# Optimization experiments

Measured on AMD Instinct MI355X. Metric: run time of the kernel, lower is better.

Reference implementation:

```python
import jax, jax.numpy as jnp
import numpy as np

BJORCK_BETA = 0.5
BJORCK_ITERS = 25

def bjorck_orthonormalize(w, iters=BJORCK_ITERS):
    # Order-2 Bjorck iteration (beta must be 0.5):
    # w <- 15/8 * w - 5/4 * w (w^T w) + 3/8 * w (w^T w)^2
    def body(i, w):
        wtw = w.T @ w                     # [out, out] on the thin side
        wtw2 = wtw @ wtw
        return 1.875 * w - 1.25 * (w @ wtw) + 0.375 * (w @ wtw2)
    return jax.lax.fori_loop(0, iters, body, w)

def setup_inputs() -> dict:
    key = jax.random.key(0)
    k1, k2, k3 = jax.random.split(key, 3)
    N, D_IN, D_OUT = 8192, 512, 256
    x = jax.random.normal(k1, (N, D_IN), dtype=jnp.float32)
    adj = jax.random.uniform(k2, (N, N), dtype=jnp.float32)
    weight = jax.random.normal(k3, (D_OUT, D_IN), dtype=jnp.float32) / np.sqrt(D_IN)
    return {"x": x, "adj": adj, "weight": weight}

def reference(x, adj, weight):
    # safe Bjorck scaling: sqrt(rows * cols) of the weight (shape-only constant)
    scaling = jnp.sqrt(jnp.float32(weight.shape[0] * weight.shape[1]))
    # orthonormalize weight.T / scaling, then transpose back -> [out, in]
    ortho_w = bjorck_orthonormalize(weight.T / scaling).T
    h = x @ ortho_w.T                      # [N, out] == F.linear(x, ortho_w)
    return jax.nn.relu(adj @ h)            # [N, out]
```

## Files before the change

### kernel.cpp

```cpp
#include <hip/hip_runtime.h>

typedef __attribute__((ext_vector_type(8))) short bf16x8;
typedef __attribute__((ext_vector_type(4))) short bf16x4;
typedef __attribute__((ext_vector_type(4))) float f32x4;

__device__ __forceinline__ unsigned short f2bf(float x){
  unsigned u = __float_as_uint(x);
  u = (u + 0x7fffu + ((u >> 16) & 1u)) >> 16;
  return (unsigned short)u;
}

__device__ __forceinline__ bf16x8 cvtpack8(float4 a, float4 b){
  union { bf16x8 v; unsigned short u[8]; } p;
  p.u[0] = f2bf(a.x); p.u[1] = f2bf(a.y); p.u[2] = f2bf(a.z); p.u[3] = f2bf(a.w);
  p.u[4] = f2bf(b.x); p.u[5] = f2bf(b.y); p.u[6] = f2bf(b.z); p.u[7] = f2bf(b.w);
  return p.v;
}

__device__ __forceinline__ void gload16(const void* g, void* l){
  __builtin_amdgcn_global_load_lds(
      (const __attribute__((address_space(1))) unsigned int*)g,
      (__attribute__((address_space(3))) unsigned int*)l, 16, 0, 0);
}


__global__ __launch_bounds__(256) void kzero(float* __restrict__ G0, float* __restrict__ n2){
  int b = blockIdx.x;
  if (b < 256) G0[b * 256 + threadIdx.x] = 0.0f;
  else if (threadIdx.x == 0) *n2 = 0.0f;
}


__global__ __launch_bounds__(256) void knorm(const float* __restrict__ wt, float* __restrict__ n2){
  int t = blockIdx.x * 256 + threadIdx.x;
  float4 v = reinterpret_cast<const float4*>(wt)[t];
  float s = v.x*v.x + v.y*v.y + v.z*v.z + v.w*v.w;
  #pragma unroll
  for (int o = 32; o > 0; o >>= 1) s += __shfl_down(s, o, 64);
  __shared__ float red[4];
  if ((threadIdx.x & 63) == 0) red[threadIdx.x >> 6] = s;
  __syncthreads();
  if (threadIdx.x == 0) atomicAdd(n2, red[0] + red[1] + red[2] + red[3]);
}

__global__ __launch_bounds__(256) void kinit(const float* __restrict__ wt, const float* __restrict__ n2,
                                             float* __restrict__ W){
  int c = blockIdx.x;
  int r = threadIdx.x;
  float s = rsqrtf(*n2) * (1.0f / 0.3f);
  W[(size_t)r * 256 + c]         = wt[(size_t)c * 512 + r] * s;
  W[(size_t)(r + 256) * 256 + c] = wt[(size_t)c * 512 + r + 256] * s;
}

__global__ __launch_bounds__(256) void kgram2(const float* __restrict__ W, float* __restrict__ G){
  __shared__ __align__(16) float Wi[64][32];
  __shared__ __align__(16) float Wj[64][32];
  const int t = threadIdx.x;
  const int i0 = blockIdx.y * 32, j0 = blockIdx.x * 32, k0 = blockIdx.z * 64;
  const int lr = t >> 3, lc = (t & 7) * 4;
  #pragma unroll
  for (int p = 0; p < 2; ++p){
    int r = lr + p * 32;
    *reinterpret_cast<float4*>(&Wi[r][lc]) =
        *reinterpret_cast<const float4*>(&W[(size_t)(k0 + r) * 256 + i0 + lc]);
    *reinterpret_cast<float4*>(&Wj[r][lc]) =
        *reinterpret_cast<const float4*>(&W[(size_t)(k0 + r) * 256 + j0 + lc]);
  }
  __syncthreads();
  const int tx = t & 31, iy = t >> 5;
  float g0 = 0, g1 = 0, g2 = 0, g3 = 0;
  #pragma unroll 8
  for (int k = 0; k < 64; ++k){
    float wj = Wj[k][tx];
    float4 wi = *reinterpret_cast<const float4*>(&Wi[k][iy * 4]);
    g0 = fmaf(wi.x, wj, g0); g1 = fmaf(wi.y, wj, g1);
    g2 = fmaf(wi.z, wj, g2); g3 = fmaf(wi.w, wj, g3);
  }
  float* gp = &G[(size_t)(i0 + iy * 4) * 256 + j0 + tx];
  atomicAdd(gp,       g0); atomicAdd(gp + 256, g1);
  atomicAdd(gp + 512, g2); atomicAdd(gp + 768, g3);
}

__global__ __launch_bounds__(512) void kupdate2(float* __restrict__ W, const float* __restrict__ G,
    float* __restrict__ Gnext, float ca, float cb, float cc, int last,
    unsigned short* __restrict__ WT2){
  __shared__ float wr[2][256], yl[2][256];
  const int t = threadIdx.x;
  const int c = t & 255, row = t >> 8;
  const int r = blockIdx.x * 2 + row;
  wr[row][c] = W[(size_t)r * 256 + c];
  __syncthreads();
  float y = 0;
  #pragma unroll 8
  for (int k = 0; k < 256; ++k)
    y = fmaf(wr[row][k], G[(size_t)k * 256 + c], y);
  yl[row][c] = y;
  __syncthreads();
  float d = 0;
  #pragma unroll 8
  for (int k = 0; k < 256; ++k)
    d = fmaf(yl[row][k], G[(size_t)k * 256 + c], d);
  float nw = ca * wr[row][c] + cb * y + cc * d;
  W[(size_t)r * 256 + c] = nw;
  if (r < 256) Gnext[(size_t)r * 256 + c] = 0.0f;
  if (last){
    size_t e = (size_t)(r >> 5) * 8192 + (size_t)((r >> 3) & 3) * 2048 + (size_t)c * 8 + (r & 7);
    WT2[e] = f2bf(nw);
  }
}


template<int KDIM, int KS, int EPI>
__global__ __launch_bounds__(256) void kgemmS(const float* __restrict__ A,
    const unsigned short* __restrict__ B, void* __restrict__ Cout){
  __shared__ __align__(16) unsigned short As[2][4096];
  __shared__ __align__(16) unsigned short Bs[2][8192];

  const int t = threadIdx.x;
  const int w = t >> 6, lane = t & 63;
  const int rlo = lane & 15, l16 = lane >> 4;
  const int kp = (KS > 1) ? (int)(blockIdx.x % KS) : 0;
  const int rb = (KS > 1) ? (int)(blockIdx.x / KS) : (int)blockIdx.x;
  constexpr int KLOC = KDIM / KS;
  constexpr int NS = KLOC / 32;
  const int kbase = kp * KLOC;

  const int arow = t >> 1, akh = t & 1;
  const float* astg = A + (size_t)(rb * 128 + arow) * KDIM + kbase + akh * 16;
  const int aswz = (arow >> 1) & 3;
  const int ab0 = arow * 64 + ((2 * akh)     ^ aswz) * 16;
  const int ab1 = arow * 64 + ((2 * akh + 1) ^ aswz) * 16;
  const unsigned short* bstg = B + (size_t)(kbase >> 5) * 8192 + w * 2048 + lane * 8;

  f32x4 acc[2][16];
  #pragma unroll
  for (int mf = 0; mf < 2; ++mf)
    #pragma unroll
    for (int nf = 0; nf < 16; ++nf){
      acc[mf][nf][0] = 0.f; acc[mf][nf][1] = 0.f;
      acc[mf][nf][2] = 0.f; acc[mf][nf][3] = 0.f;
    }

  float4 q0, q1, q2, q3;
#define LOADA(S) { const float* p_ = astg + (size_t)(S) * 32; \
    q0 = *reinterpret_cast<const float4*>(p_); \
    q1 = *reinterpret_cast<const float4*>(p_ + 4); \
    q2 = *reinterpret_cast<const float4*>(p_ + 8); \
    q3 = *reinterpret_cast<const float4*>(p_ + 12); }
#define WRITEA(BUF) { char* b_ = reinterpret_cast<char*>(&As[BUF][0]); \
    *reinterpret_cast<bf16x8*>(b_ + ab0) = cvtpack8(q0, q1); \
    *reinterpret_cast<bf16x8*>(b_ + ab1) = cvtpack8(q2, q3); }
#define STAGE_B(BUF, S) { \
    _Pragma("unroll") \
    for (int i = 0; i < 4; ++i) \
      gload16(bstg + (size_t)(S) * 8192 + i * 512, &Bs[BUF][w * 2048 + i * 512]); }
#define COMPUTE(BUF) { \
    bf16x8 afr[2]; \
    const char* ab_ = reinterpret_cast<const char*>(&As[BUF][0]); \
    _Pragma("unroll") \
    for (int mf = 0; mf < 2; ++mf){ \
      int row = w * 32 + mf * 16 + rlo; \
      afr[mf] = *reinterpret_cast<const bf16x8*>( \
          ab_ + row * 64 + ((l16 ^ ((row >> 1) & 3)) * 16)); \
    } \
    _Pragma("unroll") \
    for (int nf = 0; nf < 16; ++nf){ \
      bf16x8 bf_ = *reinterpret_cast<const bf16x8*>(&Bs[BUF][l16 * 2048 + (nf * 16 + rlo) * 8]); \
      acc[0][nf] = __builtin_amdgcn_mfma_f32_16x16x32_bf16(afr[0], bf_, acc[0][nf], 0, 0, 0); \
      acc[1][nf] = __builtin_amdgcn_mfma_f32_16x16x32_bf16(afr[1], bf_, acc[1][nf], 0, 0, 0); \
    } }

  STAGE_B(0, 0);
  LOADA(0);
  WRITEA(0);
  __syncthreads();

  #pragma unroll 1
  for (int s = 0; s < NS; ++s){
    const int cur = s & 1;
    if (s + 1 < NS){ STAGE_B(cur ^ 1, s + 1); LOADA(s + 1); }
    COMPUTE(cur);
    if (s + 1 < NS) WRITEA(cur ^ 1);
    __syncthreads();
  }
#undef LOADA
#undef WRITEA
#undef STAGE_B
#undef COMPUTE

  if constexpr (EPI == 0){
    unsigned short* H = reinterpret_cast<unsigned short*>(Cout);
    #pragma unroll
    for (int mf = 0; mf < 2; ++mf)
      #pragma unroll
      for (int nf = 0; nf < 16; ++nf){
        int c  = nf * 16 + rlo;
        int m0 = rb * 128 + w * 32 + mf * 16 + (l16 << 2);
        size_t e = (size_t)(m0 >> 5) * 8192 + (size_t)((m0 >> 3) & 3) * 2048
                 + (size_t)c * 8 + (m0 & 7);
        union { bf16x4 v; unsigned short u[4]; } p;
        p.u[0] = f2bf(acc[mf][nf][0]);
        p.u[1] = f2bf(acc[mf][nf][1]);
        p.u[2] = f2bf(acc[mf][nf][2]);
        p.u[3] = f2bf(acc[mf][nf][3]);
        *reinterpret_cast<bf16x4*>(&H[e]) = p.v;
      }
  } else {
    float* O = reinterpret_cast<float*>(Cout) + (size_t)kp * 8192 * 256;
    #pragma unroll
    for (int mf = 0; mf < 2; ++mf)
      #pragma unroll
      for (int nf = 0; nf < 16; ++nf){
        int c  = nf * 16 + rlo;
        int m0 = rb * 128 + w * 32 + mf * 16 + (l16 << 2);
        #pragma unroll
        for (int j = 0; j < 4; ++j)
          O[(size_t)(m0 + j) * 256 + c] = acc[mf][nf][j];
      }
  }
}

__global__ __launch_bounds__(256) void kreduce8(const float* __restrict__ P, float* __restrict__ O){
  size_t i = (size_t)blockIdx.x * 256 + threadIdx.x;
  const float4* p = reinterpret_cast<const float4*>(P);
  float4 r = p[i];
  #pragma unroll
  for (int q = 1; q < 8; ++q){
    float4 b = p[i + (size_t)q * 524288];
    r.x += b.x; r.y += b.y; r.z += b.z; r.w += b.w;
  }
  r.x = fmaxf(r.x, 0.f); r.y = fmaxf(r.y, 0.f);
  r.z = fmaxf(r.z, 0.f); r.w = fmaxf(r.w, 0.f);
  reinterpret_cast<float4*>(O)[i] = r;
}


extern "C" void kernel_launch(void* const* d_in, const int* in_sizes, int n_in,
                              void* d_out, int out_size, void* d_ws, size_t ws_size,
                              hipStream_t stream) {
  const float* x   = (const float*)d_in[0];
  const float* adj = (const float*)d_in[1];
  const float* wt  = (const float*)d_in[2];
  float* out = (float*)d_out;

  char* ws = (char*)d_ws;
  float* n2            = (float*)ws;
  float* W             = (float*)(ws + 4096);
  float* G0            = (float*)(ws + 4096 + 524288);
  float* G1            = (float*)(ws + 4096 + 524288 + 262144);
  unsigned short* WT2  = (unsigned short*)(ws + 4096 + 524288 + 2*262144);
  unsigned short* HT2  = (unsigned short*)(ws + 4096 + 524288 + 3*262144);
  float* Cpart         = (float*)(ws + 4096 + 524288 + 3*262144 + 4194304);

  kzero<<<257, 256, 0, stream>>>(G0, n2);
  knorm<<<128, 256, 0, stream>>>(wt, n2);
  kinit<<<256, 256, 0, stream>>>(wt, n2, W);

  const float ca[4] = { 4.2000f, 3.4445f, 1.875f, 1.875f };
  const float cb[4] = {-9.0000f, -4.7750f, -1.25f, -1.25f };
  const float cc[4] = {-6.8000f, 2.0315f, 0.375f, 0.375f };
  float* Gb[2] = {G0, G1};
  for (int it = 0; it < 4; ++it){
    float* Gc = Gb[it & 1];
    float* Gn = Gb[(it + 1) & 1];
    kgram2<<<dim3(8, 8, 8), 256, 0, stream>>>(W, Gc);
    kupdate2<<<256, 512, 0, stream>>>(W, Gc, Gn, ca[it], cb[it], cc[it], it == 3 ? 1 : 0, WT2);
  }

  kgemmS<512, 1, 0><<<64, 256, 0, stream>>>(x, WT2, (void*)HT2);
  kgemmS<8192, 8, 1><<<512, 256, 0, stream>>>(adj, HT2, (void*)Cpart);
  kreduce8<<<2048, 256, 0, stream>>>(Cpart, out);
}
```

Measured before the change: 261.9 us.

## Replace adjacency GEMM with 256-row, 512-thread triple-buffered fp32-staged kernel

Adds a new kernel for the large adj @ H product. It uses 256-row tiles with 8 waves and a 3-stage global-to-LDS pipeline. The fp32 adjacency tiles are staged directly into LDS with an XOR swizzle and converted to bf16 at fragment-load time. Larger tiles halve the block count and improve reuse of the B operand per loaded adj byte. In exchange it needs heavy LDS use (about 144KB) at one block per CU, and gives up the old kernel's layout.

```diff
diff --git a/kernel.cpp b/kernel.cpp
--- a/kernel.cpp
+++ b/kernel.cpp
@@ -108,7 +108,6 @@
     WT2[e] = f2bf(nw);
   }
 }
-
 
 template<int KDIM, int KS, int EPI>
 __global__ __launch_bounds__(256) void kgemmS(const float* __restrict__ A,
@@ -220,6 +219,98 @@
   }
 }
 
+template<int KDIM, int KS>
+__global__ __launch_bounds__(512, 1) void kgemmB(const float* __restrict__ A,
+    const unsigned short* __restrict__ B, float* __restrict__ Cout){
+  __shared__ __align__(16) float          As[3][8192];
+  __shared__ __align__(16) unsigned short Bs[3][8192];
+
+  const int t = threadIdx.x;
+  const int w = t >> 6, lane = t & 63;
+  const int rlo = lane & 15, l16 = lane >> 4;
+  const int wr = w >> 2, wc = w & 3;
+  const int kp = (int)(blockIdx.x % KS);
+  const int rb = (int)(blockIdx.x / KS);
+  constexpr int KLOC = KDIM / KS;
+  constexpr int NT = KLOC / 32;
+  const int kbase = kp * KLOC;
+
+  const int srow = lane >> 3;
+  const int sslot = (lane & 7) ^ srow;
+  const float* astg = A + (size_t)(rb * 256 + w * 32 + srow) * KDIM + kbase + sslot * 4;
+  const unsigned short* bstg = B + (size_t)(kbase >> 5) * 8192 + w * 1024 + lane * 8;
+
+  f32x4 acc[8][4];
+  #pragma unroll
+  for (int mf = 0; mf < 8; ++mf)
+    #pragma unroll
+    for (int nf = 0; nf < 4; ++nf){
+      acc[mf][nf][0] = 0.f; acc[mf][nf][1] = 0.f;
+      acc[mf][nf][2] = 0.f; acc[mf][nf][3] = 0.f;
+    }
+
+#define STAGEK(bi, st) { \
+    _Pragma("unroll") \
+    for (int i = 0; i < 4; ++i) \
+      gload16(astg + (size_t)(st) * 32 + (size_t)i * 8 * KDIM, \
+              &As[bi][(w * 32 + i * 8) * 32]); \
+    _Pragma("unroll") \
+    for (int i = 0; i < 2; ++i) \
+      gload16(bstg + (size_t)(st) * 8192 + i * 512, &Bs[bi][w * 1024 + i * 512]); }
+
+#define COMPUTEK(bi) { \
+    bf16x8 bfr[4]; \
+    _Pragma("unroll") \
+    for (int nf = 0; nf < 4; ++nf) \
+      bfr[nf] = *reinterpret_cast<const bf16x8*>( \
+          &Bs[bi][l16 * 2048 + (wc * 64 + nf * 16 + rlo) * 8]); \
+    _Pragma("unroll") \
+    for (int mf = 0; mf < 8; ++mf){ \
+      int R = wr * 128 + mf * 16 + rlo; \
+      int s0 = (l16 * 2) ^ (R & 7); \
+      int s1 = (l16 * 2 + 1) ^ (R & 7); \
+      float4 f0 = *reinterpret_cast<const float4*>(&As[bi][R * 32 + s0 * 4]); \
+      float4 f1 = *reinterpret_cast<const float4*>(&As[bi][R * 32 + s1 * 4]); \
+      bf16x8 afr = cvtpack8(f0, f1); \
+      _Pragma("unroll") \
+      for (int nf = 0; nf < 4; ++nf) \
+        acc[mf][nf] = __builtin_amdgcn_mfma_f32_16x16x32_bf16(afr, bfr[nf], acc[mf][nf], 0, 0, 0); \
+    } }
+
+  STAGEK(0, 0);
+  STAGEK(1, 1);
+  asm volatile("s_waitcnt vmcnt(6)" ::: "memory");
+  __builtin_amdgcn_s_barrier();
+  asm volatile("" ::: "memory");
+
+  int cur = 0;
+  #pragma unroll 1
+  for (int s = 0; s < NT; ++s){
+    int nb = cur + 2; if (nb >= 3) nb -= 3;
+    int st = (s + 2 < NT) ? s + 2 : NT - 1;
+    STAGEK(nb, st);
+    COMPUTEK(cur);
+    asm volatile("s_waitcnt vmcnt(6)" ::: "memory");
+    __builtin_amdgcn_s_barrier();
+    asm volatile("" ::: "memory");
+    if (++cur == 3) cur = 0;
+  }
+#undef STAGEK
+#undef COMPUTEK
+
+  float* O = Cout + (size_t)kp * 8192 * 256;
+  #pragma unroll
+  for (int mf = 0; mf < 8; ++mf)
+    #pragma unroll
+    for (int nf = 0; nf < 4; ++nf){
+      int c  = wc * 64 + nf * 16 + rlo;
+      int m0 = rb * 256 + wr * 128 + mf * 16 + (l16 << 2);
+      #pragma unroll
+      for (int j = 0; j < 4; ++j)
+        O[(size_t)(m0 + j) * 256 + c] = acc[mf][nf][j];
+    }
+}
+
 __global__ __launch_bounds__(256) void kreduce8(const float* __restrict__ P, float* __restrict__ O){
   size_t i = (size_t)blockIdx.x * 256 + threadIdx.x;
   const float4* p = reinterpret_cast<const float4*>(P);
@@ -268,6 +359,6 @@
   }
 
   kgemmS<512, 1, 0><<<64, 256, 0, stream>>>(x, WT2, (void*)HT2);
-  kgemmS<8192, 8, 1><<<512, 256, 0, stream>>>(adj, HT2, (void*)Cpart);
+  kgemmB<8192, 8><<<256, 512, 0, stream>>>(adj, HT2, Cpart);
   kreduce8<<<2048, 256, 0, stream>>>(Cpart, out);
 }
```

New measurement: 245.7 us. 1.07x faster.

## Add direct-register A-load GEMM with triple-buffered B for adjacency matmul

Applied to the files above, without the earlier changes.

Adds a new 512-thread GEMM kernel for the large adj @ h product. It loads fp32 adj rows straight into registers and converts them to bf16 in-register, skipping the LDS staging of A. B tiles are triple-buffered in LDS with asynchronous global-to-LDS loads issued two steps ahead. Each block covers 256 rows, so the grid shrinks to 256 blocks. This aims to cut LDS traffic and hide memory latency on the bandwidth-bound adj stream, at the cost of higher register pressure and fewer blocks in flight.

```diff
diff --git a/kernel.cpp b/kernel.cpp
--- a/kernel.cpp
+++ b/kernel.cpp
@@ -108,7 +108,6 @@
     WT2[e] = f2bf(nw);
   }
 }
-
 
 template<int KDIM, int KS, int EPI>
 __global__ __launch_bounds__(256) void kgemmS(const float* __restrict__ A,
@@ -220,6 +219,98 @@
   }
 }
 
+template<int KDIM, int KS>
+__global__ __launch_bounds__(512) void kgemmF(const float* __restrict__ A,
+    const unsigned short* __restrict__ B, float* __restrict__ Cout){
+  __shared__ __align__(16) unsigned short Bs[3][8192];
+
+  const int t = threadIdx.x;
+  const int w = t >> 6, lane = t & 63;
+  const int rlo = lane & 15, l16 = lane >> 4;
+  const int kp = (int)(blockIdx.x % KS);
+  const int rb = (int)(blockIdx.x / KS);
+  constexpr int KLOC = KDIM / KS;
+  constexpr int NS = KLOC / 32;
+  const int kbase = kp * KLOC;
+
+  const int row0 = rb * 256 + w * 32 + rlo;
+  const float* a0 = A + (size_t)row0 * KDIM + kbase + l16 * 8;
+  const float* a1 = a0 + (size_t)16 * KDIM;
+  const unsigned short* bstg = B + (size_t)(kbase >> 5) * 8192 + w * 1024 + lane * 8;
+
+  f32x4 acc[2][16];
+  #pragma unroll
+  for (int mf = 0; mf < 2; ++mf)
+    #pragma unroll
+    for (int nf = 0; nf < 16; ++nf){
+      acc[mf][nf][0] = 0.f; acc[mf][nf][1] = 0.f;
+      acc[mf][nf][2] = 0.f; acc[mf][nf][3] = 0.f;
+    }
+
+#define LDA(Q, S) { const float* pa_ = a0 + (size_t)(S) * 32; \
+    const float* pb_ = a1 + (size_t)(S) * 32; \
+    Q[0] = *reinterpret_cast<const float4*>(pa_); \
+    Q[1] = *reinterpret_cast<const float4*>(pa_ + 4); \
+    Q[2] = *reinterpret_cast<const float4*>(pb_); \
+    Q[3] = *reinterpret_cast<const float4*>(pb_ + 4); }
+#define STB(BUF, S) { \
+    _Pragma("unroll") \
+    for (int i = 0; i < 2; ++i) \
+      gload16(bstg + (size_t)(S) * 8192 + i * 512, &Bs[BUF][w * 1024 + i * 512]); }
+#define STEP(PB, Q, S) { \
+    bf16x8 bfr[16]; \
+    _Pragma("unroll") \
+    for (int nf = 0; nf < 16; ++nf) \
+      bfr[nf] = *reinterpret_cast<const bf16x8*>(&Bs[PB][l16 * 2048 + (nf * 16 + rlo) * 8]); \
+    bf16x8 afr0 = cvtpack8(Q[0], Q[1]); \
+    bf16x8 afr1 = cvtpack8(Q[2], Q[3]); \
+    { int st_ = ((S) + 2 < NS) ? (S) + 2 : NS - 1; \
+      int pn_ = (PB) + 2; if (pn_ >= 3) pn_ -= 3; \
+      LDA(Q, st_); \
+      STB(pn_, st_); } \
+    _Pragma("unroll") \
+    for (int nf = 0; nf < 16; ++nf){ \
+      acc[0][nf] = __builtin_amdgcn_mfma_f32_16x16x32_bf16(afr0, bfr[nf], acc[0][nf], 0, 0, 0); \
+      acc[1][nf] = __builtin_amdgcn_mfma_f32_16x16x32_bf16(afr1, bfr[nf], acc[1][nf], 0, 0, 0); \
+    } \
+    asm volatile("s_waitcnt vmcnt(6)" ::: "memory"); \
+    __builtin_amdgcn_s_barrier(); \
+    asm volatile("" ::: "memory"); }
+
+  float4 q0[4], q1[4];
+  STB(0, 0);
+  STB(1, 1);
+  LDA(q0, 0);
+  LDA(q1, 1);
+  asm volatile("s_waitcnt vmcnt(4)" ::: "memory");
+  __builtin_amdgcn_s_barrier();
+  asm volatile("" ::: "memory");
+
+  int p = 0;
+  #pragma unroll 1
+  for (int s = 0; s < NS; s += 2){
+    int p1 = p + 1; if (p1 >= 3) p1 -= 3;
+    STEP(p, q0, s);
+    STEP(p1, q1, s + 1);
+    p = p1 + 1; if (p >= 3) p -= 3;
+  }
+#undef LDA
+#undef STB
+#undef STEP
+
+  float* O = Cout + (size_t)kp * 8192 * 256;
+  #pragma unroll
+  for (int mf = 0; mf < 2; ++mf)
+    #pragma unroll
+    for (int nf = 0; nf < 16; ++nf){
+      int c  = nf * 16 + rlo;
+      int m0 = rb * 256 + w * 32 + mf * 16 + (l16 << 2);
+      #pragma unroll
+      for (int j = 0; j < 4; ++j)
+        O[(size_t)(m0 + j) * 256 + c] = acc[mf][nf][j];
+    }
+}
+
 __global__ __launch_bounds__(256) void kreduce8(const float* __restrict__ P, float* __restrict__ O){
   size_t i = (size_t)blockIdx.x * 256 + threadIdx.x;
   const float4* p = reinterpret_cast<const float4*>(P);
@@ -268,6 +359,6 @@
   }
 
   kgemmS<512, 1, 0><<<64, 256, 0, stream>>>(x, WT2, (void*)HT2);
-  kgemmS<8192, 8, 1><<<512, 256, 0, stream>>>(adj, HT2, (void*)Cpart);
+  kgemmF<8192, 8><<<256, 512, 0, stream>>>(adj, HT2, Cpart);
   kreduce8<<<2048, 256, 0, stream>>>(Cpart, out);
 }
```

Result: faster. 238.1 us (-9.1%).
